# Performance work log

Measured on AMD Instinct MI355X. Metric: run time of the kernel, lower is better.

The kernel has to match this reference:

```python
import jax, jax.numpy as jnp
import numpy as np

N, E = 20000, 320000
IN, HID, OUT, H = 128, 32, 1, 4
EPS = 1e-16  # PyG softmax epsilon


def _p(key, shape, scale=0.05):
    return jax.random.normal(key, shape, dtype=jnp.float32) * scale


def setup_inputs() -> dict:
    key = jax.random.key(0)
    ks = jax.random.split(key, 20)
    d = {
        "x": jax.random.normal(ks[0], (N, IN), dtype=jnp.float32),
        "edge_src": jax.random.randint(ks[1], (E,), 0, N, dtype=jnp.int32),
        "edge_dst": jax.random.randint(ks[2], (E,), 0, N, dtype=jnp.int32),
        # layer 1: TransformerConv(IN, HID, H)  ->  [N, H*HID]
        "W1q": _p(ks[3], (IN, H * HID)), "b1q": jnp.zeros((H * HID,), jnp.float32),
        "W1k": _p(ks[4], (IN, H * HID)), "b1k": jnp.zeros((H * HID,), jnp.float32),
        "W1v": _p(ks[5], (IN, H * HID)), "b1v": jnp.zeros((H * HID,), jnp.float32),
        "W1s": _p(ks[6], (IN, H * HID)), "b1s": jnp.zeros((H * HID,), jnp.float32),
        # layer 2: TransformerConv(H*HID, OUT, H) -> [N, H*OUT]
        "W2q": _p(ks[7], (H * HID, H * OUT)), "b2q": jnp.zeros((H * OUT,), jnp.float32),
        "W2k": _p(ks[8], (H * HID, H * OUT)), "b2k": jnp.zeros((H * OUT,), jnp.float32),
        "W2v": _p(ks[9], (H * HID, H * OUT)), "b2v": jnp.zeros((H * OUT,), jnp.float32),
        "W2s": _p(ks[10], (H * HID, H * OUT)), "b2s": jnp.zeros((H * OUT,), jnp.float32),
        # final nn.Linear(heads, 1)
        "Wl": _p(ks[11], (H, 1)), "bl": jnp.zeros((1,), jnp.float32),
    }
    return d


def transformer_conv(x, src, dst, Wq, bq, Wk, bk, Wv, bv, Ws, bs, heads, ch):
    n = x.shape[0]
    q = (x @ Wq + bq).reshape(n, heads, ch)
    k = (x @ Wk + bk).reshape(n, heads, ch)
    v = (x @ Wv + bv).reshape(n, heads, ch)
    qi, kj, vj = q[dst], k[src], v[src]            # [E,H,C] gathers
    score = (qi * kj).sum(-1) / jnp.sqrt(jnp.float32(ch))  # [E,H]
    m = jax.ops.segment_max(score, dst, num_segments=n)    # segment softmax by target
    e = jnp.exp(score - m[dst])
    s = jax.ops.segment_sum(e, dst, num_segments=n)
    alpha = e / (s[dst] + EPS)                              # [E,H]
    agg = jax.ops.segment_sum(alpha[:, :, None] * vj, dst, num_segments=n)  # [N,H,C]
    return agg.reshape(n, heads * ch) + x @ Ws + bs          # concat + root skip


def reference(x, edge_src, edge_dst,
              W1q, b1q, W1k, b1k, W1v, b1v, W1s, b1s,
              W2q, b2q, W2k, b2k, W2v, b2v, W2s, b2s,
              Wl, bl):
    h = transformer_conv(x, edge_src, edge_dst, W1q, b1q, W1k, b1k, W1v, b1v, W1s, b1s, H, HID)
    h = jax.nn.relu(h)  # dropout is identity in eval
    h = transformer_conv(h, edge_src, edge_dst, W2q, b2q, W2k, b2k, W2v, b2v, W2s, b2s, H, OUT)
    y = h @ Wl + bl                      # [N,1]
    return y.mean(axis=0, keepdims=True)  # [1,1]
```

## Files before the change

### kernel.cpp

```cpp
#include <hip/hip_runtime.h>
#include <math.h>

static constexpr float EPS_PYG = 1e-16f;
static constexpr float INV_SQRT32 = 0.17677669529663687f;

typedef short bf16x8 __attribute__((ext_vector_type(8)));
typedef float f32x4 __attribute__((ext_vector_type(4)));

__device__ inline unsigned short f2bf(float f) {
    union { float f; unsigned u; } x; x.f = f;
    unsigned r = x.u + 0x7FFFu + ((x.u >> 16) & 1u);
    return (unsigned short)(r >> 16);
}
__device__ inline float bf_hi(unsigned u) {
    union { unsigned u; float f; } x; x.u = u & 0xFFFF0000u; return x.f;
}
__device__ inline float bf_lo(unsigned u) {
    union { unsigned u; float f; } x; x.u = u << 16; return x.f;
}

__global__ __launch_bounds__(256) void build_prep_kernel(
    const int* __restrict__ dst, int* __restrict__ deg, int* __restrict__ slot,
    int E, int nblk_deg,
    const float* __restrict__ Wq, const float* __restrict__ Wk,
    const float* __restrict__ Wv, const float* __restrict__ Wsk,
    unsigned short* __restrict__ Wbt)
{
    const int b = blockIdx.x;
    const int t = threadIdx.x;
    if (b < nblk_deg) {
        int e = b * 256 + t;
        if (e < E) slot[e] = atomicAdd(&deg[dst[e]], 1);
    } else {
        int m = b - nblk_deg;
        const float* W = (m == 0) ? Wq : (m == 1) ? Wk : (m == 2) ? Wv : Wsk;
        for (int i = t; i < 16384; i += 256) {
            int k = i >> 7, nn = i & 127;
            Wbt[m * 16384 + nn * 128 + k] = f2bf(W[i]);
        }
    }
}

__global__ __launch_bounds__(1024) void scan_kernel(const int* __restrict__ deg,
                                                    int* __restrict__ row_off, int n,
                                                    float* __restrict__ out,
                                                    const float* __restrict__ bl) {
    const int t = threadIdx.x;
    const int CH = (n + 1023) >> 10;
    const int base = t * CH;
    int vals[32];
    int sum = 0;
#pragma unroll 4
    for (int i = 0; i < CH; ++i) {
        int idx = base + i;
        int v = (idx < n) ? deg[idx] : 0;
        sum += v;
        vals[i] = sum;
    }
    const int lane = t & 63;
    const int wid = t >> 6;
    int wsum = sum;
#pragma unroll
    for (int off = 1; off < 64; off <<= 1) {
        int o = __shfl_up(wsum, off, 64);
        if (lane >= off) wsum += o;
    }
    __shared__ int wtot[16];
    if (lane == 63) wtot[wid] = wsum;
    __syncthreads();
    if (t < 64) {
        int v = (t < 16) ? wtot[t] : 0;
        int inc = v;
#pragma unroll
        for (int off = 1; off < 16; off <<= 1) {
            int o = __shfl_up(inc, off, 64);
            if (t >= off) inc += o;
        }
        if (t < 16) wtot[t] = inc - v;
    }
    __syncthreads();
    const int toff = wtot[wid] + (wsum - sum);
    if (t == 0) { row_off[0] = 0; out[0] = bl[0]; }
#pragma unroll 4
    for (int i = 0; i < CH; ++i) {
        int idx = base + i;
        if (idx < n) row_off[idx + 1] = toff + vals[i];
    }
}

__global__ void scatter_kernel(const int* __restrict__ src, const int* __restrict__ dst,
                               const int* __restrict__ row_off, const int* __restrict__ slot,
                               int* __restrict__ csr_src, int E) {
    int e = blockIdx.x * blockDim.x + threadIdx.x;
    if (e < E) csr_src[row_off[dst[e]] + slot[e]] = src[e];
}

__global__ __launch_bounds__(256) void gemm1_mfma(
    const float* __restrict__ X, const unsigned short* __restrict__ Wbt,
    const float* __restrict__ bq, const float* __restrict__ bk,
    const float* __restrict__ bv, const float* __restrict__ bsk,
    unsigned int* __restrict__ QS, unsigned int* __restrict__ KV, int n)
{
    const int mode = blockIdx.y;

    const int tid  = threadIdx.x;
    const int wave = tid >> 6;
    const int lane = tid & 63;
    const int m    = lane & 15;
    const int quad = lane >> 4;
    const int r0   = blockIdx.x * 64 + wave * 16;

    int arow = r0 + m;
    if (arow >= n) arow = n - 1;

    const unsigned short* WA = Wbt + (size_t)(mode ? 1 : 0) * 16384;
    const unsigned short* WB = Wbt + (size_t)(mode ? 2 : 3) * 16384;
    const float* biasA = mode ? bk : bq;
    const float* biasB = mode ? bv : bsk;
    unsigned int* Out = mode ? KV : QS;

    const float4* xr = (const float4*)(X + (size_t)arow * 128);

    f32x4 accA[8] = {};
    f32x4 accB[8] = {};
#pragma unroll
    for (int kc = 0; kc < 128; kc += 32) {
        float4 f0 = xr[(kc >> 2) + quad * 2];
        float4 f1 = xr[(kc >> 2) + quad * 2 + 1];
        bf16x8 a;
        a[0] = (short)f2bf(f0.x); a[1] = (short)f2bf(f0.y);
        a[2] = (short)f2bf(f0.z); a[3] = (short)f2bf(f0.w);
        a[4] = (short)f2bf(f1.x); a[5] = (short)f2bf(f1.y);
        a[6] = (short)f2bf(f1.z); a[7] = (short)f2bf(f1.w);
#pragma unroll
        for (int ct = 0; ct < 8; ++ct) {
            bf16x8 ba = *(const bf16x8*)(WA + (ct * 16 + m) * 128 + kc + quad * 8);
            accA[ct] = __builtin_amdgcn_mfma_f32_16x16x32_bf16(a, ba, accA[ct], 0, 0, 0);
            bf16x8 bb = *(const bf16x8*)(WB + (ct * 16 + m) * 128 + kc + quad * 8);
            accB[ct] = __builtin_amdgcn_mfma_f32_16x16x32_bf16(a, bb, accB[ct], 0, 0, 0);
        }
    }
#pragma unroll
    for (int ct = 0; ct < 8; ++ct) {
        const int col = ct * 16 + m;
        const float bA = biasA[col], bB = biasB[col];
#pragma unroll
        for (int r = 0; r < 4; ++r) {
            const int row = r0 + quad * 4 + r;
            if (row < n) {
                unsigned ha = f2bf(accA[ct][r] + bA);
                unsigned lb = f2bf(accB[ct][r] + bB);
                Out[(size_t)row * 128 + col] = (ha << 16) | lb;
            }
        }
    }
}

__global__ __launch_bounds__(256) void l1_agg_kernel(
    const unsigned int* __restrict__ QS, const unsigned int* __restrict__ KV,
    const int* __restrict__ row_off, const int* __restrict__ csr_src,
    const float* __restrict__ W2q, const float* __restrict__ W2k,
    const float* __restrict__ W2v, const float* __restrict__ W2s,
    const float* __restrict__ b2q, const float* __restrict__ b2k,
    const float* __restrict__ b2v, const float* __restrict__ b2s,
    float4* __restrict__ Q2, float4* __restrict__ KV2, float4* __restrict__ S2,
    int n)
{
    const int t = threadIdx.x;
    const int node = blockIdx.x * 4 + (t >> 6);
    if (node >= n) return;
    const int l    = t & 31;
    const int half = (t >> 5) & 1;
    const int lf   = t & 63;
    const int cbase = ((l >> 3) << 5) + ((l & 7) << 2);

    const uint4 qs = *(const uint4*)(QS + (size_t)node * 128 + cbase);
    const float4 q = make_float4(bf_hi(qs.x), bf_hi(qs.y), bf_hi(qs.z), bf_hi(qs.w));
    const int beg = row_off[node], end = row_off[node + 1];

    float lsum = 0.f, a0 = 0.f, a1 = 0.f, a2 = 0.f, a3 = 0.f;
    int pos = beg + half;
    for (; pos + 2 < end; pos += 4) {
        int s0 = csr_src[pos];
        int s1 = csr_src[pos + 2];
        uint4 u0 = *(const uint4*)(KV + (size_t)s0 * 128 + cbase);
        uint4 u1 = *(const uint4*)(KV + (size_t)s1 * 128 + cbase);
        float p0 = q.x * bf_hi(u0.x) + q.y * bf_hi(u0.y)
                 + q.z * bf_hi(u0.z) + q.w * bf_hi(u0.w);
        float p1 = q.x * bf_hi(u1.x) + q.y * bf_hi(u1.y)
                 + q.z * bf_hi(u1.z) + q.w * bf_hi(u1.w);
        p0 += __shfl_xor(p0, 4, 8);  p1 += __shfl_xor(p1, 4, 8);
        p0 += __shfl_xor(p0, 2, 8);  p1 += __shfl_xor(p1, 2, 8);
        p0 += __shfl_xor(p0, 1, 8);  p1 += __shfl_xor(p1, 1, 8);
        float e0 = __expf(p0 * INV_SQRT32);
        float e1 = __expf(p1 * INV_SQRT32);
        lsum += e0 + e1;
        a0 += e0 * bf_lo(u0.x) + e1 * bf_lo(u1.x);
        a1 += e0 * bf_lo(u0.y) + e1 * bf_lo(u1.y);
        a2 += e0 * bf_lo(u0.z) + e1 * bf_lo(u1.z);
        a3 += e0 * bf_lo(u0.w) + e1 * bf_lo(u1.w);
    }
    if (pos < end) {
        int s0 = csr_src[pos];
        uint4 u0 = *(const uint4*)(KV + (size_t)s0 * 128 + cbase);
        float p0 = q.x * bf_hi(u0.x) + q.y * bf_hi(u0.y)
                 + q.z * bf_hi(u0.z) + q.w * bf_hi(u0.w);
        p0 += __shfl_xor(p0, 4, 8);
        p0 += __shfl_xor(p0, 2, 8);
        p0 += __shfl_xor(p0, 1, 8);
        float e0 = __expf(p0 * INV_SQRT32);
        lsum += e0;
        a0 += e0 * bf_lo(u0.x);
        a1 += e0 * bf_lo(u0.y);
        a2 += e0 * bf_lo(u0.z);
        a3 += e0 * bf_lo(u0.w);
    }
    lsum += __shfl_xor(lsum, 32, 64);
    a0   += __shfl_xor(a0,   32, 64);
    a1   += __shfl_xor(a1,   32, 64);
    a2   += __shfl_xor(a2,   32, 64);
    a3   += __shfl_xor(a3,   32, 64);

    const float inv = 1.0f / (lsum + EPS_PYG);
    const float h0 = fmaxf(a0 * inv + bf_lo(qs.x), 0.f);
    const float h1 = fmaxf(a1 * inv + bf_lo(qs.y), 0.f);
    const float h2 = fmaxf(a2 * inv + bf_lo(qs.z), 0.f);
    const float h3 = fmaxf(a3 * inv + bf_lo(qs.w), 0.f);

    const float* WA = half ? W2v : W2q;
    const float* WB = half ? W2s : W2k;
    float p0, p1, p2, p3, p4, p5, p6, p7;
    {
        float4 wa = *(const float4*)(WA + (size_t)(cbase + 0) * 4);
        float4 wb = *(const float4*)(WB + (size_t)(cbase + 0) * 4);
        p0 = h0 * wa.x; p1 = h0 * wa.y; p2 = h0 * wa.z; p3 = h0 * wa.w;
        p4 = h0 * wb.x; p5 = h0 * wb.y; p6 = h0 * wb.z; p7 = h0 * wb.w;
        wa = *(const float4*)(WA + (size_t)(cbase + 1) * 4);
        wb = *(const float4*)(WB + (size_t)(cbase + 1) * 4);
        p0 += h1 * wa.x; p1 += h1 * wa.y; p2 += h1 * wa.z; p3 += h1 * wa.w;
        p4 += h1 * wb.x; p5 += h1 * wb.y; p6 += h1 * wb.z; p7 += h1 * wb.w;
        wa = *(const float4*)(WA + (size_t)(cbase + 2) * 4);
        wb = *(const float4*)(WB + (size_t)(cbase + 2) * 4);
        p0 += h2 * wa.x; p1 += h2 * wa.y; p2 += h2 * wa.z; p3 += h2 * wa.w;
        p4 += h2 * wb.x; p5 += h2 * wb.y; p6 += h2 * wb.z; p7 += h2 * wb.w;
        wa = *(const float4*)(WA + (size_t)(cbase + 3) * 4);
        wb = *(const float4*)(WB + (size_t)(cbase + 3) * 4);
        p0 += h3 * wa.x; p1 += h3 * wa.y; p2 += h3 * wa.z; p3 += h3 * wa.w;
        p4 += h3 * wb.x; p5 += h3 * wb.y; p6 += h3 * wb.z; p7 += h3 * wb.w;
    }
#pragma unroll
    for (int mk = 16; mk >= 1; mk >>= 1) {
        p0 += __shfl_xor(p0, mk, 32); p1 += __shfl_xor(p1, mk, 32);
        p2 += __shfl_xor(p2, mk, 32); p3 += __shfl_xor(p3, mk, 32);
        p4 += __shfl_xor(p4, mk, 32); p5 += __shfl_xor(p5, mk, 32);
        p6 += __shfl_xor(p6, mk, 32); p7 += __shfl_xor(p7, mk, 32);
    }
    if (lf == 0) {
        const float4 ba = *(const float4*)b2q;
        const float4 bb = *(const float4*)b2k;
        Q2[node] = make_float4(p0 + ba.x, p1 + ba.y, p2 + ba.z, p3 + ba.w);
        KV2[(size_t)node * 2 + 0] =
            make_float4(p4 + bb.x, p5 + bb.y, p6 + bb.z, p7 + bb.w);
    } else if (lf == 32) {
        const float4 ba = *(const float4*)b2v;
        const float4 bb = *(const float4*)b2s;
        KV2[(size_t)node * 2 + 1] =
            make_float4(p0 + ba.x, p1 + ba.y, p2 + ba.z, p3 + ba.w);
        S2[node] = make_float4(p4 + bb.x, p5 + bb.y, p6 + bb.z, p7 + bb.w);
    }
}

__global__ __launch_bounds__(256) void l2_agg_kernel(
    const float4* __restrict__ Q2, const float4* __restrict__ KV2,
    const float4* __restrict__ S2,
    const int* __restrict__ row_off, const int* __restrict__ csr_src,
    const float* __restrict__ Wl, float* __restrict__ out, int n, float invn)
{
    const int t  = threadIdx.x;
    const int g  = t >> 4;
    const int gl = t & 15;
    const int nd = blockIdx.x * 16 + g;
    float y = 0.f;
    if (nd < n) {
        const int beg = row_off[nd], end = row_off[nd + 1];
        float4 q = Q2[nd];
        float l0 = 0.f, l1 = 0.f, l2 = 0.f, l3 = 0.f;
        float a0 = 0.f, a1 = 0.f, a2 = 0.f, a3 = 0.f;
        for (int pos = beg + gl; pos < end; pos += 16) {
            int src = csr_src[pos];
            float4 k = KV2[(size_t)src * 2 + 0];
            float4 v = KV2[(size_t)src * 2 + 1];
            float e0 = __expf(q.x * k.x);
            float e1 = __expf(q.y * k.y);
            float e2 = __expf(q.z * k.z);
            float e3 = __expf(q.w * k.w);
            l0 += e0; a0 += e0 * v.x;
            l1 += e1; a1 += e1 * v.y;
            l2 += e2; a2 += e2 * v.z;
            l3 += e3; a3 += e3 * v.w;
        }
#pragma unroll
        for (int mk = 8; mk >= 1; mk >>= 1) {
            l0 += __shfl_xor(l0, mk, 16); l1 += __shfl_xor(l1, mk, 16);
            l2 += __shfl_xor(l2, mk, 16); l3 += __shfl_xor(l3, mk, 16);
            a0 += __shfl_xor(a0, mk, 16); a1 += __shfl_xor(a1, mk, 16);
            a2 += __shfl_xor(a2, mk, 16); a3 += __shfl_xor(a3, mk, 16);
        }
        if (gl == 0) {
            float4 sk = S2[nd];
            float h0 = a0 / (l0 + EPS_PYG) + sk.x;
            float h1 = a1 / (l1 + EPS_PYG) + sk.y;
            float h2 = a2 / (l2 + EPS_PYG) + sk.z;
            float h3 = a3 / (l3 + EPS_PYG) + sk.w;
            y = (h0 * Wl[0] + h1 * Wl[1] + h2 * Wl[2] + h3 * Wl[3]) * invn;
        }
    }
    __shared__ float red[256];
    red[t] = y;
    __syncthreads();
    for (int off = 128; off > 0; off >>= 1) {
        if (t < (unsigned)off) red[t] += red[t + off];
        __syncthreads();
    }
    if (t == 0) atomicAdd(out, red[0]);
}

extern "C" void kernel_launch(void* const* d_in, const int* in_sizes, int n_in,
                              void* d_out, int out_size, void* d_ws, size_t ws_size,
                              hipStream_t stream) {
    const float* x        = (const float*)d_in[0];
    const int*   edge_src = (const int*)d_in[1];
    const int*   edge_dst = (const int*)d_in[2];
    const float* W1q = (const float*)d_in[3];  const float* b1q = (const float*)d_in[4];
    const float* W1k = (const float*)d_in[5];  const float* b1k = (const float*)d_in[6];
    const float* W1v = (const float*)d_in[7];  const float* b1v = (const float*)d_in[8];
    const float* W1s = (const float*)d_in[9];  const float* b1s = (const float*)d_in[10];
    const float* W2q = (const float*)d_in[11]; const float* b2q = (const float*)d_in[12];
    const float* W2k = (const float*)d_in[13]; const float* b2k = (const float*)d_in[14];
    const float* W2v = (const float*)d_in[15]; const float* b2v = (const float*)d_in[16];
    const float* W2s = (const float*)d_in[17]; const float* b2s = (const float*)d_in[18];
    const float* Wl  = (const float*)d_in[19]; const float* bl  = (const float*)d_in[20];

    const int N = in_sizes[0] / 128;
    const int E = in_sizes[1];
    float* out = (float*)d_out;

    float* ws  = (float*)d_ws;
    size_t off = 0;
    unsigned int* QS  = (unsigned int*)(ws + off); off += (size_t)N * 128;
    unsigned int* KV  = (unsigned int*)(ws + off); off += (size_t)N * 128;
    float*        q2  = ws + off; off += (size_t)N * 4;
    float*        kv2 = ws + off; off += (size_t)N * 8;
    float*        s2  = ws + off; off += (size_t)N * 4;
    unsigned short* Wbt = (unsigned short*)(ws + off); off += 4 * 16384 / 2;
    int* ibase   = (int*)(ws + off);
    int* deg     = ibase;
    int* row_off = ibase + N;
    int* slot    = ibase + 2 * N + 4;
    int* csr_src = slot + E;

    const int nblk_e = (E + 255) / 256;
    const int nblk_g = (N + 63) / 64;

    hipMemsetAsync(deg, 0, (size_t)N * sizeof(int), stream);
    build_prep_kernel<<<nblk_e + 4, 256, 0, stream>>>(
        edge_dst, deg, slot, E, nblk_e, W1q, W1k, W1v, W1s, Wbt);
    scan_kernel<<<1, 1024, 0, stream>>>(deg, row_off, N, out, bl);
    scatter_kernel<<<nblk_e, 256, 0, stream>>>(edge_src, edge_dst, row_off,
                                               slot, csr_src, E);
    {
        dim3 grid(nblk_g, 2);
        gemm1_mfma<<<grid, 256, 0, stream>>>(x, Wbt, b1q, b1k, b1v, b1s,
                                             QS, KV, N);
    }
    l1_agg_kernel<<<(N + 3) / 4, 256, 0, stream>>>(
        QS, KV, row_off, csr_src, W2q, W2k, W2v, W2s, b2q, b2k, b2v, b2s,
        (float4*)q2, (float4*)kv2, (float4*)s2, N);
    l2_agg_kernel<<<(N + 15) / 16, 256, 0, stream>>>((const float4*)q2,
                                                     (const float4*)kv2,
                                                     (const float4*)s2,
                                                     row_off, csr_src, Wl, out, N,
                                                     1.0f / (float)N);
}
```

Measured before the change: 232.6 us.

## Fuse CSR build into one cooperative kernel with grid syncs; unroll l1 agg loop

```diff
diff --git a/kernel.cpp b/kernel.cpp
--- a/kernel.cpp
+++ b/kernel.cpp
@@ -1,8 +1,13 @@
 #include <hip/hip_runtime.h>
+#include <hip/hip_cooperative_groups.h>
 #include <math.h>
+
+namespace cg = cooperative_groups;
 
 static constexpr float EPS_PYG = 1e-16f;
 static constexpr float INV_SQRT32 = 0.17677669529663687f;
+static constexpr int GBLK = 512;
+static constexpr int CHUNK = 64;
 
 typedef short bf16x8 __attribute__((ext_vector_type(8)));
 typedef float f32x4 __attribute__((ext_vector_type(4)));
@@ -19,80 +24,83 @@
     union { unsigned u; float f; } x; x.u = u << 16; return x.f;
 }
 
-__global__ __launch_bounds__(256) void build_prep_kernel(
-    const int* __restrict__ dst, int* __restrict__ deg, int* __restrict__ slot,
-    int E, int nblk_deg,
+__global__ __launch_bounds__(256) void csr_coop_kernel(
+    const int* __restrict__ src, const int* __restrict__ dst,
+    int E, int N,
     const float* __restrict__ Wq, const float* __restrict__ Wk,
     const float* __restrict__ Wv, const float* __restrict__ Wsk,
-    unsigned short* __restrict__ Wbt)
+    unsigned short* __restrict__ Wbt,
+    int* __restrict__ deg, int* __restrict__ slot,
+    int* __restrict__ lofs, int* __restrict__ bsum, int* __restrict__ boff,
+    int* __restrict__ row_off, int* __restrict__ csr_src,
+    float* __restrict__ out, const float* __restrict__ bl)
 {
+    cg::grid_group grid = cg::this_grid();
+    const int t = threadIdx.x;
     const int b = blockIdx.x;
-    const int t = threadIdx.x;
-    if (b < nblk_deg) {
-        int e = b * 256 + t;
-        if (e < E) slot[e] = atomicAdd(&deg[dst[e]], 1);
-    } else {
-        int m = b - nblk_deg;
+    const int gid = b * 256 + t;
+    const int GT = GBLK * 256;
+
+    for (int i = gid; i < N; i += GT) deg[i] = 0;
+    for (int j = gid; j < 4 * 16384; j += GT) {
+        int m = j >> 14, i = j & 16383;
+        int k = i >> 7, nn = i & 127;
         const float* W = (m == 0) ? Wq : (m == 1) ? Wk : (m == 2) ? Wv : Wsk;
-        for (int i = t; i < 16384; i += 256) {
-            int k = i >> 7, nn = i & 127;
-            Wbt[m * 16384 + nn * 128 + k] = f2bf(W[i]);
-        }
-    }
-}
-
-__global__ __launch_bounds__(1024) void scan_kernel(const int* __restrict__ deg,
-                                                    int* __restrict__ row_off, int n,
-                                                    float* __restrict__ out,
-                                                    const float* __restrict__ bl) {
-    const int t = threadIdx.x;
-    const int CH = (n + 1023) >> 10;
-    const int base = t * CH;
-    int vals[32];
-    int sum = 0;
-#pragma unroll 4
-    for (int i = 0; i < CH; ++i) {
-        int idx = base + i;
-        int v = (idx < n) ? deg[idx] : 0;
-        sum += v;
-        vals[i] = sum;
-    }
-    const int lane = t & 63;
-    const int wid = t >> 6;
-    int wsum = sum;
-#pragma unroll
-    for (int off = 1; off < 64; off <<= 1) {
-        int o = __shfl_up(wsum, off, 64);
-        if (lane >= off) wsum += o;
-    }
-    __shared__ int wtot[16];
-    if (lane == 63) wtot[wid] = wsum;
-    __syncthreads();
-    if (t < 64) {
-        int v = (t < 16) ? wtot[t] : 0;
-        int inc = v;
-#pragma unroll
-        for (int off = 1; off < 16; off <<= 1) {
-            int o = __shfl_up(inc, off, 64);
-            if (t >= off) inc += o;
-        }
-        if (t < 16) wtot[t] = inc - v;
-    }
-    __syncthreads();
-    const int toff = wtot[wid] + (wsum - sum);
-    if (t == 0) { row_off[0] = 0; out[0] = bl[0]; }
-#pragma unroll 4
-    for (int i = 0; i < CH; ++i) {
-        int idx = base + i;
-        if (idx < n) row_off[idx + 1] = toff + vals[i];
-    }
-}
-
-__global__ void scatter_kernel(const int* __restrict__ src, const int* __restrict__ dst,
-                               const int* __restrict__ row_off, const int* __restrict__ slot,
-                               int* __restrict__ csr_src, int E) {
-    int e = blockIdx.x * blockDim.x + threadIdx.x;
-    if (e < E) csr_src[row_off[dst[e]] + slot[e]] = src[e];
+        Wbt[(m << 14) + nn * 128 + k] = f2bf(W[i]);
+    }
+    grid.sync();
+
+    for (int e = gid; e < E; e += GT) slot[e] = atomicAdd(&deg[dst[e]], 1);
+    grid.sync();
+
+    {
+        const int base = b * CHUNK;
+        if (t < 64) {
+            int idx = base + t;
+            int v = (idx < N) ? deg[idx] : 0;
+            int s = v;
+#pragma unroll
+            for (int off = 1; off < 64; off <<= 1) {
+                int o = __shfl_up(s, off, 64);
+                if (t >= off) s += o;
+            }
+            if (idx < N) lofs[idx] = s;
+            if (t == 63) bsum[b] = s;
+        }
+    }
+    grid.sync();
+
+    if (b == 0) {
+        if (t < 64) {
+            int acc[GBLK / 64];
+            int sum = 0;
+#pragma unroll
+            for (int i = 0; i < GBLK / 64; ++i) {
+                int v = bsum[t * (GBLK / 64) + i];
+                acc[i] = sum; sum += v;
+            }
+            int s = sum;
+#pragma unroll
+            for (int off = 1; off < 64; off <<= 1) {
+                int o = __shfl_up(s, off, 64);
+                if (t >= off) s += o;
+            }
+            int excl = s - sum;
+#pragma unroll
+            for (int i = 0; i < GBLK / 64; ++i)
+                boff[t * (GBLK / 64) + i] = excl + acc[i];
+        }
+        if (t == 0) { row_off[0] = 0; out[0] = bl[0]; }
+    }
+    grid.sync();
+
+    for (int i = gid; i < N; i += GT)
+        row_off[i + 1] = boff[i >> 6] + lofs[i];
+    for (int e = gid; e < E; e += GT) {
+        int d = dst[e];
+        int ro = boff[d >> 6] + lofs[d] - deg[d];
+        csr_src[ro + slot[e]] = src[e];
+    }
 }
 
 __global__ __launch_bounds__(256) void gemm1_mfma(
@@ -180,6 +188,43 @@
 
     float lsum = 0.f, a0 = 0.f, a1 = 0.f, a2 = 0.f, a3 = 0.f;
     int pos = beg + half;
+    for (; pos + 6 < end; pos += 8) {
+        int s0 = csr_src[pos];
+        int s1 = csr_src[pos + 2];
+        int s2 = csr_src[pos + 4];
+        int s3 = csr_src[pos + 6];
+        uint4 u0 = *(const uint4*)(KV + (size_t)s0 * 128 + cbase);
+        uint4 u1 = *(const uint4*)(KV + (size_t)s1 * 128 + cbase);
+        uint4 u2 = *(const uint4*)(KV + (size_t)s2 * 128 + cbase);
+        uint4 u3 = *(const uint4*)(KV + (size_t)s3 * 128 + cbase);
+        float p0 = q.x * bf_hi(u0.x) + q.y * bf_hi(u0.y)
+                 + q.z * bf_hi(u0.z) + q.w * bf_hi(u0.w);
+        float p1 = q.x * bf_hi(u1.x) + q.y * bf_hi(u1.y)
+                 + q.z * bf_hi(u1.z) + q.w * bf_hi(u1.w);
+        float p2 = q.x * bf_hi(u2.x) + q.y * bf_hi(u2.y)
+                 + q.z * bf_hi(u2.z) + q.w * bf_hi(u2.w);
+        float p3 = q.x * bf_hi(u3.x) + q.y * bf_hi(u3.y)
+                 + q.z * bf_hi(u3.z) + q.w * bf_hi(u3.w);
+        p0 += __shfl_xor(p0, 4, 8);  p1 += __shfl_xor(p1, 4, 8);
+        p2 += __shfl_xor(p2, 4, 8);  p3 += __shfl_xor(p3, 4, 8);
+        p0 += __shfl_xor(p0, 2, 8);  p1 += __shfl_xor(p1, 2, 8);
+        p2 += __shfl_xor(p2, 2, 8);  p3 += __shfl_xor(p3, 2, 8);
+        p0 += __shfl_xor(p0, 1, 8);  p1 += __shfl_xor(p1, 1, 8);
+        p2 += __shfl_xor(p2, 1, 8);  p3 += __shfl_xor(p3, 1, 8);
+        float e0 = __expf(p0 * INV_SQRT32);
+        float e1 = __expf(p1 * INV_SQRT32);
+        float e2 = __expf(p2 * INV_SQRT32);
+        float e3 = __expf(p3 * INV_SQRT32);
+        lsum += (e0 + e1) + (e2 + e3);
+        a0 += e0 * bf_lo(u0.x) + e1 * bf_lo(u1.x)
+            + e2 * bf_lo(u2.x) + e3 * bf_lo(u3.x);
+        a1 += e0 * bf_lo(u0.y) + e1 * bf_lo(u1.y)
+            + e2 * bf_lo(u2.y) + e3 * bf_lo(u3.y);
+        a2 += e0 * bf_lo(u0.z) + e1 * bf_lo(u1.z)
+            + e2 * bf_lo(u2.z) + e3 * bf_lo(u3.z);
+        a3 += e0 * bf_lo(u0.w) + e1 * bf_lo(u1.w)
+            + e2 * bf_lo(u2.w) + e3 * bf_lo(u3.w);
+    }
     for (; pos + 2 < end; pos += 4) {
         int s0 = csr_src[pos];
         int s1 = csr_src[pos + 2];
@@ -341,8 +386,8 @@
     const float* W2s = (const float*)d_in[17]; const float* b2s = (const float*)d_in[18];
     const float* Wl  = (const float*)d_in[19]; const float* bl  = (const float*)d_in[20];
 
-    const int N = in_sizes[0] / 128;
-    const int E = in_sizes[1];
+    int N = in_sizes[0] / 128;
+    int E = in_sizes[1];
     float* out = (float*)d_out;
 
     float* ws  = (float*)d_ws;
@@ -356,18 +401,24 @@
     int* ibase   = (int*)(ws + off);
     int* deg     = ibase;
     int* row_off = ibase + N;
-    int* slot    = ibase + 2 * N + 4;
+    int* lofs    = ibase + 2 * N + 4;
+    int* bsum    = ibase + 3 * N + 4;
+    int* boff    = ibase + 3 * N + 4 + GBLK;
+    int* slot    = ibase + 3 * N + 4 + 2 * GBLK;
     int* csr_src = slot + E;
 
-    const int nblk_e = (E + 255) / 256;
     const int nblk_g = (N + 63) / 64;
 
-    hipMemsetAsync(deg, 0, (size_t)N * sizeof(int), stream);
-    build_prep_kernel<<<nblk_e + 4, 256, 0, stream>>>(
-        edge_dst, deg, slot, E, nblk_e, W1q, W1k, W1v, W1s, Wbt);
-    scan_kernel<<<1, 1024, 0, stream>>>(deg, row_off, N, out, bl);
-    scatter_kernel<<<nblk_e, 256, 0, stream>>>(edge_src, edge_dst, row_off,
-                                               slot, csr_src, E);
+    {
+        void* args[] = {
+            (void*)&edge_src, (void*)&edge_dst, (void*)&E, (void*)&N,
+            (void*)&W1q, (void*)&W1k, (void*)&W1v, (void*)&W1s, (void*)&Wbt,
+            (void*)&deg, (void*)&slot, (void*)&lofs, (void*)&bsum, (void*)&boff,
+            (void*)&row_off, (void*)&csr_src, (void*)&out, (void*)&bl
+        };
+        hipLaunchCooperativeKernel((const void*)csr_coop_kernel,
+                                   dim3(GBLK), dim3(256), args, 0, stream);
+    }
     {
         dim3 grid(nblk_g, 2);
         gemm1_mfma<<<grid, 256, 0, stream>>>(x, Wbt, b1q, b1k, b1v, b1s,
```

Result: slower. 436.6 us (+87.7%).
